# Optimization experiments

Hardware: AMD Instinct MI355X
Metric: run time of the kernel (lower is better)

The kernel has to match this reference:

```python
import jax, jax.numpy as jnp
from jax import lax
import numpy as np

B, T, UNITS, OUT_STEPS, NUM_FEAT, BINS, DF = 512, 1024, 256, 32, 32, 32, 15

# Acklam rational approximation of the inverse normal CDF (numpy, only used to
# build the constant Student-t quantile boundaries, replacing scipy.stats.t.ppf).
def _norm_ppf(p):
    p = np.asarray(p, dtype=np.float64)
    a = [-3.969683028665376e+01, 2.209460984245205e+02, -2.759285104469687e+02,
         1.383577518672690e+02, -3.066479806614716e+01, 2.506628277459239e+00]
    b = [-5.447609879822406e+01, 1.615858368580409e+02, -1.556989798598866e+02,
         6.680131188771972e+01, -1.328068155288572e+01]
    c = [-7.784894002430293e-03, -3.223964580411365e-01, -2.400758277161838e+00,
         -2.549732539343734e+00, 4.374664141464968e+00, 2.938163982698783e+00]
    d = [7.784695709041462e-03, 3.224671290700398e-01, 2.445134137142996e+00,
         3.754408661907416e+00]
    x = np.empty_like(p)
    lo, hi = 0.02425, 1.0 - 0.02425
    m = p < lo
    q = np.sqrt(-2.0 * np.log(p[m]))
    x[m] = (((((c[0]*q+c[1])*q+c[2])*q+c[3])*q+c[4])*q+c[5]) / ((((d[0]*q+d[1])*q+d[2])*q+d[3])*q+1.0)
    m = (p >= lo) & (p <= hi)
    q = p[m] - 0.5
    r = q * q
    x[m] = (((((a[0]*r+a[1])*r+a[2])*r+a[3])*r+a[4])*r+a[5])*q / (((((b[0]*r+b[1])*r+b[2])*r+b[3])*r+b[4])*r+1.0)
    m = p > hi
    q = np.sqrt(-2.0 * np.log(1.0 - p[m]))
    x[m] = -(((((c[0]*q+c[1])*q+c[2])*q+c[3])*q+c[4])*q+c[5]) / ((((d[0]*q+d[1])*q+d[2])*q+d[3])*q+1.0)
    return x

# Cornish-Fisher expansion of the Student-t inverse CDF around the normal quantile.
def _t_ppf(p, df):
    z = _norm_ppf(p)
    g1 = (z**3 + z) / 4.0
    g2 = (5*z**5 + 16*z**3 + 3*z) / 96.0
    g3 = (3*z**7 + 19*z**5 + 17*z**3 - 15*z) / 384.0
    g4 = (79*z**9 + 776*z**7 + 1482*z**5 - 1920*z**3 - 945*z) / 92160.0
    return z + g1/df + g2/df**2 + g3/df**3 + g4/df**4

_T_BASE = _t_ppf(np.linspace(0.0001, 0.9999, BINS - 1), DF).astype(np.float32)  # [BINS-1]


def _lstm_step(kernel, rec_kernel, bias, h, c, x):
    # Keras LSTMCell: gate order i|f|g|o, sigmoid gates, tanh cell activation.
    z = x @ kernel + h @ rec_kernel + bias
    i, f, g, o = jnp.split(z, 4, axis=-1)
    c = jax.nn.sigmoid(f) * c + jax.nn.sigmoid(i) * jnp.tanh(g)
    h = jax.nn.sigmoid(o) * jnp.tanh(c)
    return h, c


def reference(inputs, kernel, rec_kernel, bias, dense_w, dense_b):
    mu = jnp.mean(inputs, axis=1, keepdims=True)    # [B,1,1]
    sigma = jnp.std(inputs, axis=1, keepdims=True)  # [B,1,1] population std (tf.reduce_std)
    base = jnp.asarray(_T_BASE)                     # [BINS-1]
    bounds = base[None, :] * sigma[:, 0, 0, None] + mu[:, 0, 0, None]  # [B,BINS-1], sorted
    x = inputs[:, :, 0]                             # [B,T]
    # Vectorized bucketization (replaces tf.map_fn + tft.apply_buckets).
    idx = jax.vmap(lambda xb, bb: jnp.searchsorted(bb, xb, side='right'))(x, bounds)  # [B,T]
    hist = jax.nn.one_hot(idx, BINS, dtype=inputs.dtype)  # [B,T,BINS]

    units = kernel.shape[1] // 4
    h0 = jnp.zeros((x.shape[0], units), inputs.dtype)

    def enc(carry, xt):
        h, c = _lstm_step(kernel, rec_kernel, bias, carry[0], carry[1], xt)
        return (h, c), None

    (h, c), _ = lax.scan(enc, (h0, h0), hist.transpose(1, 0, 2))  # warmup over T steps
    pred = jax.nn.softmax(h @ dense_w + dense_b)                   # [B,NUM_FEAT]

    def dec(carry, _):
        h, c, p = carry
        h, c = _lstm_step(kernel, rec_kernel, bias, h, c, p)
        p = jax.nn.softmax(h @ dense_w + dense_b)
        return (h, c, p), p

    _, rest = lax.scan(dec, (h, c, pred), None, length=OUT_STEPS - 1)
    preds = jnp.concatenate([pred[None], rest], axis=0)  # [OUT_STEPS,B,F]
    preds = preds.transpose(1, 0, 2)[:, :, None, :]      # [B,OUT_STEPS,1,F]
    return preds, mu, sigma


def setup_inputs():
    key = jax.random.key(0)
    ks = jax.random.split(key, 4)
    return {
        "inputs": jax.random.normal(ks[0], (B, T, 1), jnp.float32),
        "kernel": jax.random.normal(ks[1], (BINS, 4 * UNITS), jnp.float32) * 0.1,
        "rec_kernel": jax.random.normal(ks[2], (UNITS, 4 * UNITS), jnp.float32) * 0.1,
        "bias": jnp.zeros((4 * UNITS,), jnp.float32),
        "dense_w": jax.random.normal(ks[3], (UNITS, NUM_FEAT), jnp.float32) * 0.1,
        "dense_b": jnp.zeros((NUM_FEAT,), jnp.float32),
    }
```

## Files before the change

kernel.cpp:

```cpp
#include <hip/hip_runtime.h>
#include <math.h>

#define TT      1024
#define BATCH   512
#define UNITSN  256
#define ZDIM    1024
#define NFEAT   32
#define OSTEPS  32
#define NBND    31
#define OUT_MU  (BATCH*OSTEPS*NFEAT)
#define OUT_SG  (OUT_MU + BATCH)

#define NQR     18
#define NQL     14
#define HQS     36
#define HQ(buf,row,reg) ((((buf)*2+(row))*2+(reg))*HQS)

typedef _Float16 v2h __attribute__((ext_vector_type(2)));
union UH2 { unsigned int u; v2h h; };
__device__ __forceinline__ float sigm(float x)  { return 1.0f / (1.0f + __expf(-x)); }
__device__ __forceinline__ float ftanh(float x) { float e = __expf(2.0f * x); return 1.0f - 2.0f / (e + 1.0f); }

__device__ __forceinline__ int dot4i8(unsigned int a, unsigned int b, int c) {
#if __has_builtin(__builtin_amdgcn_sdot4)
    return __builtin_amdgcn_sdot4((int)a, (int)b, c, false);
#else
    int r = c;
    #pragma unroll
    for (int i = 0; i < 4; ++i)
        r += (int)(signed char)(a >> (8*i)) * (int)(signed char)(b >> (8*i));
    return r;
#endif
}

__global__ void k_tbase(float* __restrict__ tb) {
    int i = threadIdx.x;
    if (i >= NBND) return;
    double step = (0.9999 - 0.0001) / 30.0;
    double p = 0.0001 + (double)i * step;
    if (i == 30) p = 0.9999;

    const double a0=-39.69683028665376, a1=220.9460984245205, a2=-275.9285104469687,
                 a3=138.357751867269,   a4=-30.66479806614716, a5=2.506628277459239;
    const double b0=-54.47609879822406, b1=161.5858368580409, b2=-155.6989798598866,
                 b3=66.80131188771972,  b4=-13.28068155288572;
    const double c0=-0.007784894002430293, c1=-0.3223964580411365, c2=-2.400758277161838,
                 c3=-2.549732539343734,    c4=4.374664141464968,   c5=2.938163982698783;
    const double d0=0.007784695709041462,  d1=0.3224671290700398,  d2=2.445134137142996,
                 d3=3.754408661907416;
    const double lo = 0.02425, hi = 1.0 - 0.02425;
    double z;
    if (p < lo) {
        double q = sqrt(-2.0 * log(p));
        z = (((((c0*q+c1)*q+c2)*q+c3)*q+c4)*q+c5) / ((((d0*q+d1)*q+d2)*q+d3)*q+1.0);
    } else if (p <= hi) {
        double q = p - 0.5;
        double r = q*q;
        z = (((((a0*r+a1)*r+a2)*r+a3)*r+a4)*r+a5)*q /
            (((((b0*r+b1)*r+b2)*r+b3)*r+b4)*r+1.0);
    } else {
        double q = sqrt(-2.0 * log(1.0 - p));
        z = -((((((c0*q+c1)*q+c2)*q+c3)*q+c4)*q+c5) / ((((d0*q+d1)*q+d2)*q+d3)*q+1.0));
    }
    double z2=z*z, z3=z2*z, z5=z3*z2, z7=z5*z2, z9=z7*z2;
    double g1=(z3+z)/4.0;
    double g2=(5.0*z5+16.0*z3+3.0*z)/96.0;
    double g3=(3.0*z7+19.0*z5+17.0*z3-15.0*z)/384.0;
    double g4=(79.0*z9+776.0*z7+1482.0*z5-1920.0*z3-945.0*z)/92160.0;
    const double df = 15.0;
    double t = z + g1/df + g2/(df*df) + g3/(df*df*df) + g4/(df*df*df*df);
    tb[i] = (float)t;
}

__global__ __launch_bounds__(1024)
void k_musig(const float* __restrict__ x, float* __restrict__ out,
             float* __restrict__ muv, float* __restrict__ sgv) {
    int b = blockIdx.x;
    int t = threadIdx.x;
    __shared__ float red[16];
    __shared__ float sMu;
    float v = x[(size_t)b * TT + t];

    float s = v;
    #pragma unroll
    for (int o = 32; o >= 1; o >>= 1) s += __shfl_xor(s, o, 64);
    int wid = t >> 6, lane = t & 63;
    if (lane == 0) red[wid] = s;
    __syncthreads();
    if (t == 0) {
        float tot = 0.f;
        for (int w = 0; w < 16; ++w) tot += red[w];
        sMu = tot * (1.0f / 1024.0f);
    }
    __syncthreads();
    float mu = sMu;
    float d = v - mu;
    s = d * d;
    #pragma unroll
    for (int o = 32; o >= 1; o >>= 1) s += __shfl_xor(s, o, 64);
    if (lane == 0) red[wid] = s;
    __syncthreads();
    if (t == 0) {
        float tot = 0.f;
        for (int w = 0; w < 16; ++w) tot += red[w];
        float sg = sqrtf(tot * (1.0f / 1024.0f));
        out[OUT_MU + b] = mu;
        out[OUT_SG + b] = sg;
        muv[b] = mu;
        sgv[b] = sg;
    }
}

__global__ __launch_bounds__(256)
void k_scales(const float* __restrict__ Rec, float* __restrict__ SW,
              float* __restrict__ SInv) {
    int j = blockIdx.x * 256 + threadIdx.x;
    float m = 0.f;
    for (int k = 0; k < 256; ++k) m = fmaxf(m, fabsf(Rec[(size_t)k * ZDIM + j]));
    SW[j]   = m * (1.0f / 16129.0f);
    SInv[j] = (m > 0.f) ? (127.0f / m) : 0.f;
}

__global__ __launch_bounds__(256)
void k_packQ(const float* __restrict__ Rec, const float* __restrict__ SInv,
             uint4* __restrict__ Q) {
    int e = blockIdx.x * 256 + threadIdx.x;
    int s = e >> 9, t = e & 511;
    int u = t >> 1, kh = t & 1;
    int k0 = kh * 128 + s * 4;
    unsigned int d[4];
    #pragma unroll
    for (int g = 0; g < 4; ++g) {
        int j = g * 256 + u;
        float inv = SInv[j];
        unsigned int dw = 0;
        #pragma unroll
        for (int i = 0; i < 4; ++i) {
            int q = __float2int_rn(Rec[(size_t)(k0 + i) * ZDIM + j] * inv);
            dw |= ((unsigned int)(q & 0xff)) << (8 * i);
        }
        d[g] = dw;
    }
    Q[e] = make_uint4(d[0], d[1], d[2], d[3]);
}

__global__ __launch_bounds__(256)
void k_packK(const float* __restrict__ Kmat, const float* __restrict__ Bias,
             float* __restrict__ KB) {
    int e = blockIdx.x * 256 + threadIdx.x;
    int i = e >> 10, c = e & 1023;
    int u = c >> 2, g = c & 3;
    int j = g * 256 + u;
    KB[e] = Kmat[(size_t)i * ZDIM + j] + Bias[j];
}

__global__ __launch_bounds__(512)
void k_lstm11(const float* __restrict__ x,
              const uint4* __restrict__ Q,
              const float* __restrict__ SW,
              const float* __restrict__ KB,
              const float* __restrict__ Dw,
              const float* __restrict__ Db,
              const float* __restrict__ tb,
              const float* __restrict__ muv,
              const float* __restrict__ sgv,
              float* __restrict__ out)
{
    __shared__ uint4 sWq[NQL * 512];
    __shared__ unsigned int sHq[2 * 2 * 2 * HQS];
    __shared__ float sHT[UNITSN][2];
    __shared__ unsigned char sIdx[2][TT];
    __shared__ float sBnd[2][32];
    __shared__ float sPT[NFEAT][2];
    __shared__ float sLog[2][NFEAT];

    const int tid = threadIdx.x;
    const int u   = tid >> 1;
    const int kh  = tid & 1;
    const int b0  = blockIdx.x * 2;

    if (tid < 64) {
        int rr = tid >> 5, j = tid & 31;
        if (j < NBND) sBnd[rr][j] = tb[j] * sgv[b0 + rr] + muv[b0 + rr];
    }
    if (tid < 2 * 2 * 2 * HQS) sHq[tid] = 0u;
    if (tid < UNITSN * 2) ((float*)sHT)[tid] = 0.f;

    uint4 Wreg[NQR];
    #pragma unroll
    for (int j = 0; j < NQR; ++j) {
        uint4 w = Q[j * 512 + tid];
        asm volatile("" : "+v"(w.x), "+v"(w.y), "+v"(w.z), "+v"(w.w));
        Wreg[j] = w;
    }
    #pragma unroll
    for (int l = 0; l < NQL; ++l)
        sWq[l * 512 + tid] = Q[(NQR + l) * 512 + tid];

    float4 SW4 = make_float4(SW[u], SW[256 + u], SW[512 + u], SW[768 + u]);

    for (int e = tid; e < 2 * TT; e += 512) {
        int rr = e >> 10, t = e & 1023;
        float xv = x[(size_t)(b0 + rr) * TT + t];
        int id = 0;
        #pragma unroll
        for (int q = 0; q < NBND; ++q) id += (sBnd[rr][q] <= xv) ? 1 : 0;
        sIdx[rr][t] = (unsigned char)id;
    }
    __syncthreads();

    float cC = 0.f;
    int cur = 0;
    const int wbyte_reg = u >> 7;
    const int wbyte_off = u & 127;

    auto stepCore = [&](float4 kbSelf) {
        const unsigned int* hb0 = &sHq[HQ(cur, 0, kh)];
        const unsigned int* hb1 = &sHq[HQ(cur, 1, kh)];
        int4 A0 = {0, 0, 0, 0}, A1 = {0, 0, 0, 0};
        #pragma unroll
        for (int s4 = 0; s4 < 8; ++s4) {
            uint4 hh0 = *(const uint4*)(hb0 + s4 * 4);
            uint4 hh1 = *(const uint4*)(hb1 + s4 * 4);
            #pragma unroll
            for (int i = 0; i < 4; ++i) {
                const int j = s4 * 4 + i;
                uint4 w = (j < NQR) ? Wreg[(j < NQR) ? j : 0]
                                    : sWq[(j - NQR) * 512 + tid];
                unsigned int h0 = (i==0)?hh0.x:(i==1)?hh0.y:(i==2)?hh0.z:hh0.w;
                unsigned int h1 = (i==0)?hh1.x:(i==1)?hh1.y:(i==2)?hh1.z:hh1.w;
                A0.x = dot4i8(h0, w.x, A0.x); A0.y = dot4i8(h0, w.y, A0.y);
                A0.z = dot4i8(h0, w.z, A0.z); A0.w = dot4i8(h0, w.w, A0.w);
                A1.x = dot4i8(h1, w.x, A1.x); A1.y = dot4i8(h1, w.y, A1.y);
                A1.z = dot4i8(h1, w.z, A1.z); A1.w = dot4i8(h1, w.w, A1.w);
            }
        }
        A0.x += __shfl_xor(A0.x, 1); A0.y += __shfl_xor(A0.y, 1);
        A0.z += __shfl_xor(A0.z, 1); A0.w += __shfl_xor(A0.w, 1);
        A1.x += __shfl_xor(A1.x, 1); A1.y += __shfl_xor(A1.y, 1);
        A1.z += __shfl_xor(A1.z, 1); A1.w += __shfl_xor(A1.w, 1);
        int qi = kh ? A1.x : A0.x;
        int qf = kh ? A1.y : A0.y;
        int qg = kh ? A1.z : A0.z;
        int qo = kh ? A1.w : A0.w;
        float zi = (float)qi * SW4.x + kbSelf.x;
        float zf = (float)qf * SW4.y + kbSelf.y;
        float zg = (float)qg * SW4.z + kbSelf.z;
        float zo = (float)qo * SW4.w + kbSelf.w;
        cC = sigm(zf) * cC + sigm(zi) * ftanh(zg);
        float hv = sigm(zo) * ftanh(cC);
        sHT[u][kh] = hv;
        int qh = __float2int_rn(hv * 127.0f);
        ((unsigned char*)sHq)[(HQ(cur ^ 1, kh, wbyte_reg) << 2) + wbyte_off] =
            (unsigned char)qh;
        cur ^= 1;
        __syncthreads();
    };

    auto softmaxStore = [&](int s) {
        if (tid < 64) {
            int rr = tid >> 5, f = tid & 31;
            float acc = Db[f];
            #pragma unroll 4
            for (int uu = 0; uu < UNITSN; ++uu) acc = fmaf(sHT[uu][rr], Dw[uu * NFEAT + f], acc);
            sLog[rr][f] = acc;
        }
        __syncthreads();
        if (tid < 2) {
            int rr = tid;
            float m = sLog[rr][0];
            for (int f = 1; f < NFEAT; ++f) m = fmaxf(m, sLog[rr][f]);
            float ssum = 0.f;
            for (int f = 0; f < NFEAT; ++f) {
                float e = __expf(sLog[rr][f] - m);
                sLog[rr][f] = e;
                ssum += e;
            }
            float inv = 1.0f / ssum;
            for (int f = 0; f < NFEAT; ++f) {
                float p = sLog[rr][f] * inv;
                sPT[f][rr] = p;
                out[((size_t)(b0 + rr) * OSTEPS + s) * NFEAT + f] = p;
            }
        }
        __syncthreads();
    };

    float4 kb = *(const float4*)&KB[((int)sIdx[kh][0] << 10) + (u << 2)];
    #pragma unroll 1
    for (int t = 0; t < TT; ++t) {
        float4 kb_next;
        if (t + 1 < TT)
            kb_next = *(const float4*)&KB[((int)sIdx[kh][t + 1] << 10) + (u << 2)];
        stepCore(kb);
        kb = kb_next;
    }
    softmaxStore(0);

    #pragma unroll 1
    for (int s = 1; s < OSTEPS; ++s) {
        float4 a0 = make_float4(0.f, 0.f, 0.f, 0.f), a1 = a0;
        #pragma unroll
        for (int ii = 0; ii < 16; ++ii) {
            int i = kh * 16 + ii;
            float4 w = *(const float4*)&KB[(i << 10) + (u << 2)];
            float p0 = sPT[i][0], p1 = sPT[i][1];
            a0.x = fmaf(p0, w.x, a0.x); a0.y = fmaf(p0, w.y, a0.y);
            a0.z = fmaf(p0, w.z, a0.z); a0.w = fmaf(p0, w.w, a0.w);
            a1.x = fmaf(p1, w.x, a1.x); a1.y = fmaf(p1, w.y, a1.y);
            a1.z = fmaf(p1, w.z, a1.z); a1.w = fmaf(p1, w.w, a1.w);
        }
        a0.x += __shfl_xor(a0.x, 1); a0.y += __shfl_xor(a0.y, 1);
        a0.z += __shfl_xor(a0.z, 1); a0.w += __shfl_xor(a0.w, 1);
        a1.x += __shfl_xor(a1.x, 1); a1.y += __shfl_xor(a1.y, 1);
        a1.z += __shfl_xor(a1.z, 1); a1.w += __shfl_xor(a1.w, 1);
        float4 kbSelf = (kh == 0) ? a0 : a1;
        stepCore(kbSelf);
        softmaxStore(s);
    }
}

extern "C" void kernel_launch(void* const* d_in, const int* in_sizes, int n_in,
                              void* d_out, int out_size, void* d_ws, size_t ws_size,
                              hipStream_t stream) {
    const float* inputs = (const float*)d_in[0];
    const float* kernel = (const float*)d_in[1];
    const float* rec    = (const float*)d_in[2];
    const float* bias   = (const float*)d_in[3];
    const float* dw     = (const float*)d_in[4];
    const float* db     = (const float*)d_in[5];
    float* out = (float*)d_out;

    float* tbp  = (float*)d_ws;
    float* muv  = tbp + 64;
    float* sgv  = muv + BATCH;
    float* SW   = (float*)((char*)d_ws + 4352);
    float* SInv = (float*)((char*)d_ws + 8448);
    uint4* Q    = (uint4*)((char*)d_ws + 12544);
    float* KB   = (float*)((char*)d_ws + 12544 + 262144);

    k_tbase<<<1, 32, 0, stream>>>(tbp);
    k_musig<<<BATCH, 1024, 0, stream>>>(inputs, out, muv, sgv);
    k_scales<<<4, 256, 0, stream>>>(rec, SW, SInv);
    k_packQ<<<64, 256, 0, stream>>>(rec, SInv, Q);
    k_packK<<<128, 256, 0, stream>>>(kernel, bias, KB);
    k_lstm11<<<BATCH / 2, 512, 0, stream>>>(inputs, Q, SW, KB, dw, db,
                                            tbp, muv, sgv, out);
}
```

Measured before the change: 2.093 ms.

## Split recurrent int8 dot product across four threads per unit with 1024-thread blocks

The K dimension of each hidden unit's recurrent matrix-vector product is now split across four threads instead of two. Blocks grow to 1024 threads, and the per-thread int8 weight slice drops to 7 register plus 9 LDS uint4 chunks. Partial sums are combined with an extra xor-2 shuffle stage, and only two of the four lanes run the gate math and write h. The aim is to shorten the serial dot-product chain on each timestep of the latency-bound recurrence. The costs are a larger LDS footprint, heavier 1024-thread barriers, and the loss of the next-step KB prefetch, so the input-projection load now sits on the critical path.

Measured after the change: 2.728 ms. +30.3%, slower.

```diff
diff --git a/kernel.cpp b/kernel.cpp
--- a/kernel.cpp
+++ b/kernel.cpp
@@ -11,13 +11,11 @@
 #define OUT_MU  (BATCH*OSTEPS*NFEAT)
 #define OUT_SG  (OUT_MU + BATCH)
 
-#define NQR     18
-#define NQL     14
-#define HQS     36
-#define HQ(buf,row,reg) ((((buf)*2+(row))*2+(reg))*HQS)
-
-typedef _Float16 v2h __attribute__((ext_vector_type(2)));
-union UH2 { unsigned int u; v2h h; };
+#define NQR     7
+#define NQL     9
+#define HQS4    20
+#define HQ4(buf,row,reg) ((((buf)*2+(row))*4+(reg))*HQS4)
+
 __device__ __forceinline__ float sigm(float x)  { return 1.0f / (1.0f + __expf(-x)); }
 __device__ __forceinline__ float ftanh(float x) { float e = __expf(2.0f * x); return 1.0f - 2.0f / (e + 1.0f); }
 
@@ -122,12 +120,12 @@
 }
 
 __global__ __launch_bounds__(256)
-void k_packQ(const float* __restrict__ Rec, const float* __restrict__ SInv,
-             uint4* __restrict__ Q) {
+void k_packQ4(const float* __restrict__ Rec, const float* __restrict__ SInv,
+              uint4* __restrict__ Q) {
     int e = blockIdx.x * 256 + threadIdx.x;
-    int s = e >> 9, t = e & 511;
-    int u = t >> 1, kh = t & 1;
-    int k0 = kh * 128 + s * 4;
+    int s = e >> 10, t = e & 1023;
+    int u = t >> 2, kq = t & 3;
+    int k0 = kq * 64 + s * 4;
     unsigned int d[4];
     #pragma unroll
     for (int g = 0; g < 4; ++g) {
@@ -154,8 +152,8 @@
     KB[e] = Kmat[(size_t)i * ZDIM + j] + Bias[j];
 }
 
-__global__ __launch_bounds__(512)
-void k_lstm11(const float* __restrict__ x,
+__global__ __launch_bounds__(1024)
+void k_lstm12(const float* __restrict__ x,
               const uint4* __restrict__ Q,
               const float* __restrict__ SW,
               const float* __restrict__ KB,
@@ -166,8 +164,8 @@
               const float* __restrict__ sgv,
               float* __restrict__ out)
 {
-    __shared__ uint4 sWq[NQL * 512];
-    __shared__ unsigned int sHq[2 * 2 * 2 * HQS];
+    __shared__ uint4 sWq[NQL * 1024];
+    __shared__ unsigned int sHq[2 * 2 * 4 * HQS4];
     __shared__ float sHT[UNITSN][2];
     __shared__ unsigned char sIdx[2][TT];
     __shared__ float sBnd[2][32];
@@ -175,31 +173,31 @@
     __shared__ float sLog[2][NFEAT];
 
     const int tid = threadIdx.x;
-    const int u   = tid >> 1;
-    const int kh  = tid & 1;
+    const int u   = tid >> 2;
+    const int kq  = tid & 3;
     const int b0  = blockIdx.x * 2;
 
     if (tid < 64) {
         int rr = tid >> 5, j = tid & 31;
         if (j < NBND) sBnd[rr][j] = tb[j] * sgv[b0 + rr] + muv[b0 + rr];
     }
-    if (tid < 2 * 2 * 2 * HQS) sHq[tid] = 0u;
+    if (tid < 2 * 2 * 4 * HQS4) sHq[tid] = 0u;
     if (tid < UNITSN * 2) ((float*)sHT)[tid] = 0.f;
 
     uint4 Wreg[NQR];
     #pragma unroll
     for (int j = 0; j < NQR; ++j) {
-        uint4 w = Q[j * 512 + tid];
+        uint4 w = Q[j * 1024 + tid];
         asm volatile("" : "+v"(w.x), "+v"(w.y), "+v"(w.z), "+v"(w.w));
         Wreg[j] = w;
     }
     #pragma unroll
     for (int l = 0; l < NQL; ++l)
-        sWq[l * 512 + tid] = Q[(NQR + l) * 512 + tid];
+        sWq[l * 1024 + tid] = Q[(NQR + l) * 1024 + tid];
 
     float4 SW4 = make_float4(SW[u], SW[256 + u], SW[512 + u], SW[768 + u]);
 
-    for (int e = tid; e < 2 * TT; e += 512) {
+    for (int e = tid; e < 2 * TT; e += 1024) {
         int rr = e >> 10, t = e & 1023;
         float xv = x[(size_t)(b0 + rr) * TT + t];
         int id = 0;
@@ -211,22 +209,23 @@
 
     float cC = 0.f;
     int cur = 0;
-    const int wbyte_reg = u >> 7;
-    const int wbyte_off = u & 127;
+    const int wreg_idx = u >> 6;
+    const int wreg_off = u & 63;
 
     auto stepCore = [&](float4 kbSelf) {
-        const unsigned int* hb0 = &sHq[HQ(cur, 0, kh)];
-        const unsigned int* hb1 = &sHq[HQ(cur, 1, kh)];
+        const unsigned int* hb0 = &sHq[HQ4(cur, 0, kq)];
+        const unsigned int* hb1 = &sHq[HQ4(cur, 1, kq)];
         int4 A0 = {0, 0, 0, 0}, A1 = {0, 0, 0, 0};
         #pragma unroll
-        for (int s4 = 0; s4 < 8; ++s4) {
+        for (int s4 = 0; s4 < 4; ++s4) {
             uint4 hh0 = *(const uint4*)(hb0 + s4 * 4);
             uint4 hh1 = *(const uint4*)(hb1 + s4 * 4);
             #pragma unroll
             for (int i = 0; i < 4; ++i) {
                 const int j = s4 * 4 + i;
-                uint4 w = (j < NQR) ? Wreg[(j < NQR) ? j : 0]
-                                    : sWq[(j - NQR) * 512 + tid];
+                uint4 w;
+                if (j < NQR) w = Wreg[j < NQR ? j : 0];
+                else         w = sWq[(j - NQR) * 1024 + tid];
                 unsigned int h0 = (i==0)?hh0.x:(i==1)?hh0.y:(i==2)?hh0.z:hh0.w;
                 unsigned int h1 = (i==0)?hh1.x:(i==1)?hh1.y:(i==2)?hh1.z:hh1.w;
                 A0.x = dot4i8(h0, w.x, A0.x); A0.y = dot4i8(h0, w.y, A0.y);
@@ -239,20 +238,26 @@
         A0.z += __shfl_xor(A0.z, 1); A0.w += __shfl_xor(A0.w, 1);
         A1.x += __shfl_xor(A1.x, 1); A1.y += __shfl_xor(A1.y, 1);
         A1.z += __shfl_xor(A1.z, 1); A1.w += __shfl_xor(A1.w, 1);
-        int qi = kh ? A1.x : A0.x;
-        int qf = kh ? A1.y : A0.y;
-        int qg = kh ? A1.z : A0.z;
-        int qo = kh ? A1.w : A0.w;
-        float zi = (float)qi * SW4.x + kbSelf.x;
-        float zf = (float)qf * SW4.y + kbSelf.y;
-        float zg = (float)qg * SW4.z + kbSelf.z;
-        float zo = (float)qo * SW4.w + kbSelf.w;
-        cC = sigm(zf) * cC + sigm(zi) * ftanh(zg);
-        float hv = sigm(zo) * ftanh(cC);
-        sHT[u][kh] = hv;
-        int qh = __float2int_rn(hv * 127.0f);
-        ((unsigned char*)sHq)[(HQ(cur ^ 1, kh, wbyte_reg) << 2) + wbyte_off] =
-            (unsigned char)qh;
+        A0.x += __shfl_xor(A0.x, 2); A0.y += __shfl_xor(A0.y, 2);
+        A0.z += __shfl_xor(A0.z, 2); A0.w += __shfl_xor(A0.w, 2);
+        A1.x += __shfl_xor(A1.x, 2); A1.y += __shfl_xor(A1.y, 2);
+        A1.z += __shfl_xor(A1.z, 2); A1.w += __shfl_xor(A1.w, 2);
+        if (kq < 2) {
+            int qi = kq ? A1.x : A0.x;
+            int qf = kq ? A1.y : A0.y;
+            int qg = kq ? A1.z : A0.z;
+            int qo = kq ? A1.w : A0.w;
+            float zi = (float)qi * SW4.x + kbSelf.x;
+            float zf = (float)qf * SW4.y + kbSelf.y;
+            float zg = (float)qg * SW4.z + kbSelf.z;
+            float zo = (float)qo * SW4.w + kbSelf.w;
+            cC = sigm(zf) * cC + sigm(zi) * ftanh(zg);
+            float hv = sigm(zo) * ftanh(cC);
+            sHT[u][kq] = hv;
+            int qh = __float2int_rn(hv * 127.0f);
+            ((unsigned char*)sHq)[(HQ4(cur ^ 1, kq, wreg_idx) << 2) + wreg_off] =
+                (unsigned char)qh;
+        }
         cur ^= 1;
         __syncthreads();
     };
@@ -286,14 +291,12 @@
         __syncthreads();
     };
 
-    float4 kb = *(const float4*)&KB[((int)sIdx[kh][0] << 10) + (u << 2)];
     #pragma unroll 1
     for (int t = 0; t < TT; ++t) {
-        float4 kb_next;
-        if (t + 1 < TT)
-            kb_next = *(const float4*)&KB[((int)sIdx[kh][t + 1] << 10) + (u << 2)];
+        float4 kb = make_float4(0.f, 0.f, 0.f, 0.f);
+        if (kq < 2)
+            kb = *(const float4*)&KB[((int)sIdx[kq][t] << 10) + (u << 2)];
         stepCore(kb);
-        kb = kb_next;
     }
     softmaxStore(0);
 
@@ -301,8 +304,8 @@
     for (int s = 1; s < OSTEPS; ++s) {
         float4 a0 = make_float4(0.f, 0.f, 0.f, 0.f), a1 = a0;
         #pragma unroll
-        for (int ii = 0; ii < 16; ++ii) {
-            int i = kh * 16 + ii;
+        for (int ii = 0; ii < 8; ++ii) {
+            int i = kq * 8 + ii;
             float4 w = *(const float4*)&KB[(i << 10) + (u << 2)];
             float p0 = sPT[i][0], p1 = sPT[i][1];
             a0.x = fmaf(p0, w.x, a0.x); a0.y = fmaf(p0, w.y, a0.y);
@@ -314,7 +317,11 @@
         a0.z += __shfl_xor(a0.z, 1); a0.w += __shfl_xor(a0.w, 1);
         a1.x += __shfl_xor(a1.x, 1); a1.y += __shfl_xor(a1.y, 1);
         a1.z += __shfl_xor(a1.z, 1); a1.w += __shfl_xor(a1.w, 1);
-        float4 kbSelf = (kh == 0) ? a0 : a1;
+        a0.x += __shfl_xor(a0.x, 2); a0.y += __shfl_xor(a0.y, 2);
+        a0.z += __shfl_xor(a0.z, 2); a0.w += __shfl_xor(a0.w, 2);
+        a1.x += __shfl_xor(a1.x, 2); a1.y += __shfl_xor(a1.y, 2);
+        a1.z += __shfl_xor(a1.z, 2); a1.w += __shfl_xor(a1.w, 2);
+        float4 kbSelf = (kq == 0) ? a0 : a1;
         stepCore(kbSelf);
         softmaxStore(s);
     }
@@ -342,8 +349,8 @@
     k_tbase<<<1, 32, 0, stream>>>(tbp);
     k_musig<<<BATCH, 1024, 0, stream>>>(inputs, out, muv, sgv);
     k_scales<<<4, 256, 0, stream>>>(rec, SW, SInv);
-    k_packQ<<<64, 256, 0, stream>>>(rec, SInv, Q);
+    k_packQ4<<<64, 256, 0, stream>>>(rec, SInv, Q);
     k_packK<<<128, 256, 0, stream>>>(kernel, bias, KB);
-    k_lstm11<<<BATCH / 2, 512, 0, stream>>>(inputs, Q, SW, KB, dw, db,
-                                            tbp, muv, sgv, out);
-}
+    k_lstm12<<<BATCH / 2, 1024, 0, stream>>>(inputs, Q, SW, KB, dw, db,
+                                             tbp, muv, sgv, out);
+}
```
